# Kernel optimization log

Measured on AMD Instinct MI355X. Metric: run time of the kernel, lower is better.

## Reference

```python
import jax, jax.numpy as jnp
import numpy as np

G = 131072      # number of agent groups (batched graphs)
N_AGENTS = 6    # 5 search parties + 1 helicopter, fully-connected graph per group
D_IN = 64       # input_dim
H = 64          # hidden_dim (conv1 out)
GH = 64         # gnn_hidden (conv2 out, MLP hidden)
OUT = 2         # actor action dim
N_TYPES = 2     # agent types: search party (0), helicopter (1)


def setup_inputs() -> dict:
    key = jax.random.key(0)
    ks = jax.random.split(key, 20)
    s = 0.05
    inp = {
        'obs': jax.random.normal(ks[0], (G, N_AGENTS, D_IN), jnp.float32),
        # SAGEConv('pool') layer 1: fc_pool (in->in), fc_self, fc_neigh, bias
        'Wp1': jax.random.normal(ks[1], (D_IN, D_IN), jnp.float32) * s,
        'bp1': jnp.zeros((D_IN,), jnp.float32),
        'Ws1': jax.random.normal(ks[2], (D_IN, H), jnp.float32) * s,
        'Wn1': jax.random.normal(ks[3], (D_IN, H), jnp.float32) * s,
        'b1': jnp.zeros((H,), jnp.float32),
        # SAGEConv('pool') layer 2
        'Wp2': jax.random.normal(ks[4], (H, H), jnp.float32) * s,
        'bp2': jnp.zeros((H,), jnp.float32),
        'Ws2': jax.random.normal(ks[5], (H, GH), jnp.float32) * s,
        'Wn2': jax.random.normal(ks[6], (H, GH), jnp.float32) * s,
        'b2': jnp.zeros((GH,), jnp.float32),
        # per-agent-type actor MLPs (stacked over type axis t=2)
        'MW1': jax.random.normal(ks[7], (N_TYPES, GH, GH), jnp.float32) * s,
        'Mb1': jnp.zeros((N_TYPES, GH), jnp.float32),
        'MW2': jax.random.normal(ks[8], (N_TYPES, GH, GH), jnp.float32) * s,
        'Mb2': jnp.zeros((N_TYPES, GH), jnp.float32),
        'MW3': jax.random.normal(ks[9], (N_TYPES, GH, GH), jnp.float32) * s,
        'Mb3': jnp.zeros((N_TYPES, GH), jnp.float32),
        'MW4': jax.random.uniform(ks[10], (N_TYPES, GH, OUT), jnp.float32, -0.003, 0.003),
        'Mb4': jnp.zeros((N_TYPES, OUT), jnp.float32),
    }
    return inp


def _sage_pool(x, Wp, bp, Ws, Wn, b):
    # DGL SAGEConv aggregator_type='pool' on a fully-connected graph w/ self loops:
    # neigh_j = max_i relu(fc_pool(x_i)); rst = fc_self(x) + fc_neigh(neigh) + bias
    p = jax.nn.relu(x @ Wp + bp)              # [G, n, din]
    neigh = p.max(axis=1, keepdims=True)      # [G, 1, din] (all nodes are neighbors)
    return x @ Ws + neigh @ Wn + b            # [G, n, dout]


def reference(obs, Wp1, bp1, Ws1, Wn1, b1, Wp2, bp2, Ws2, Wn2, b2,
              MW1, Mb1, MW2, Mb2, MW3, Mb3, MW4, Mb4):
    h = jnp.tanh(_sage_pool(obs, Wp1, bp1, Ws1, Wn1, b1))   # conv1 + Tanh activation
    h = _sage_pool(h, Wp2, bp2, Ws2, Wn2, b2)               # conv2 (no activation)
    res = h.mean(axis=1)                                     # AvgPooling per graph -> [G, GH]
    # per-agent-type MLPs, batched over type axis t
    x = jax.nn.relu(jnp.einsum('gd,tdh->tgh', res, MW1) + Mb1[:, None, :])
    x = jax.nn.relu(jnp.einsum('tgh,thk->tgk', x, MW2) + Mb2[:, None, :])
    x = jax.nn.relu(jnp.einsum('tgh,thk->tgk', x, MW3) + Mb3[:, None, :])
    out_t = jnp.tanh(jnp.einsum('tgh,tho->tgo', x, MW4) + Mb4[:, None, :])  # [T, G, 2]
    agent_types = jnp.array([0, 0, 0, 0, 0, 1])  # 5 search parties + 1 helicopter
    return jnp.transpose(out_t[agent_types], (1, 0, 2))     # [G, 6, 2]
```

## Files before the change

### kernel.cpp

```cpp
#include <hip/hip_runtime.h>
#include <math.h>


typedef _Float16 f16;
typedef _Float16 half8_t __attribute__((ext_vector_type(8)));
typedef float    float4_t __attribute__((ext_vector_type(4)));

#define NW 8
#define SLABF (16*68)
#define LDS_PAD_F 17920

__device__ __forceinline__ int swz_off(int n, int k) {
    return n * 64 + (((k >> 3) ^ (n & 7)) << 3) + (k & 7);
}

__device__ __forceinline__ float fast_tanh(float x) {
    float e = __expf(2.0f * x);
    return 1.0f - 2.0f / (e + 1.0f);
}

__device__ __forceinline__ float4_t max4(float4_t a, float4_t b) {
    float4_t r;
    r[0] = fmaxf(a[0], b[0]); r[1] = fmaxf(a[1], b[1]);
    r[2] = fmaxf(a[2], b[2]); r[3] = fmaxf(a[3], b[3]);
    return r;
}

__device__ __forceinline__ float4_t bcast4(float v) {
    float4_t r; r[0] = v; r[1] = v; r[2] = v; r[3] = v; return r;
}

__global__ void prep_weights(const float* __restrict__ Wp1, const float* __restrict__ Ws1,
                             const float* __restrict__ Wn1, const float* __restrict__ Wp2,
                             const float* __restrict__ Ws2, const float* __restrict__ Wn2,
                             const float* __restrict__ MW1, const float* __restrict__ MW2,
                             const float* __restrict__ MW3, const float* __restrict__ MW4,
                             f16* __restrict__ img)
{
    const int m = blockIdx.x;
    const int tid = threadIdx.x;
    if (m < 12) {
        const float* src;
        switch (m) {
            case 0: src = Wp1; break;  case 1: src = Ws1; break;
            case 2: src = Wn1; break;  case 3: src = Wp2; break;
            case 4: src = Ws2; break;  case 5: src = Wn2; break;
            case 6: src = MW1; break;  case 7: src = MW2; break;
            case 8: src = MW3; break;  case 9: src = MW1 + 4096; break;
            case 10: src = MW2 + 4096; break; default: src = MW3 + 4096; break;
        }
        for (int e = tid; e < 4096; e += 256) {
            const int k = e >> 6, n = e & 63;
            img[m * 4096 + swz_off(n, k)] = (f16)src[e];
        }
    } else {
        for (int e = tid; e < 2048; e += 256) {
            const int ty = e >> 10, rem = e & 1023;
            const int n = rem >> 6, k = rem & 63;
            float v = 0.f;
            if (ty == 0) { if (n < 10) v = MW4[k * 2 + (n & 1)]; }
            else         { if (n == 10 || n == 11) v = MW4[128 + k * 2 + (n & 1)]; }
            img[12 * 4096 + ty * 1024 + swz_off(n, k)] = (f16)v;
        }
    }
}

__global__ __launch_bounds__(512, 2)
void gnn_mfma(const float* __restrict__ obs, const f16* __restrict__ img,
              const float* __restrict__ bp1, const float* __restrict__ b1,
              const float* __restrict__ bp2, const float* __restrict__ b2,
              const float* __restrict__ Mb1, const float* __restrict__ Mb2,
              const float* __restrict__ Mb3, const float* __restrict__ Mb4,
              float* __restrict__ out)
{
    __shared__ __align__(16) float smem[LDS_PAD_F];

    const int tid  = threadIdx.x;
    const int w    = __builtin_amdgcn_readfirstlane(tid >> 6);
    const int l    = tid & 63;
    const int col  = l & 15;
    const int quad = l >> 4;
    float* slab = smem + w * SLABF;

    if (tid == 0) {
        volatile float* guard = smem + NW * SLABF;
        guard[0] = 0.f;
    }

    auto loadB = [&](int baseH, int nt, int kf) -> half8_t {
        const int n = nt * 16 + col;
        const unsigned off = (unsigned)(baseH + n * 64 + (((kf * 4 + quad) ^ (n & 7)) << 3));
        return *(const half8_t*)(img + off);
    };
    auto loadA = [&](int kf) -> half8_t {
        const float4_t x = *(const float4_t*)(slab + col * 68 + kf * 32 + quad * 8);
        const float4_t y = *(const float4_t*)(slab + col * 68 + kf * 32 + quad * 8 + 4);
        half8_t r;
        r[0] = (f16)x[0]; r[1] = (f16)x[1]; r[2] = (f16)x[2]; r[3] = (f16)x[3];
        r[4] = (f16)y[0]; r[5] = (f16)y[1]; r[6] = (f16)y[2]; r[7] = (f16)y[3];
        return r;
    };
    auto storeC = [&](const float4_t v, int nt) {
        #pragma unroll
        for (int r = 0; r < 4; ++r)
            slab[(quad * 4 + r) * 68 + nt * 16 + col] = v[r];
    };

    float bp1v[4], b1v[4], bp2v[4], b2v[4];
    #pragma unroll
    for (int nt = 0; nt < 4; ++nt) {
        bp1v[nt] = bp1[nt * 16 + col];
        b1v[nt]  = b1[nt * 16 + col];
        bp2v[nt] = bp2[nt * 16 + col];
        b2v[nt]  = b2[nt * 16 + col];
    }
    const float mb4v = (col < 10) ? Mb4[col & 1] : Mb4[2 + (col & 1)];

    const int wid = blockIdx.x * NW + w;
    const int g0  = wid * 16;

    half8_t Aobs[6][2];
    const float* orow = obs + ((size_t)(g0 + col) * 6) * 64 + quad * 8;
    #pragma unroll
    for (int a = 0; a < 6; ++a) {
        #pragma unroll
        for (int kf = 0; kf < 2; ++kf) {
            const float4_t x = *(const float4_t*)(orow + a * 64 + kf * 32);
            const float4_t y = *(const float4_t*)(orow + a * 64 + kf * 32 + 4);
            half8_t r;
            r[0] = (f16)x[0]; r[1] = (f16)x[1]; r[2] = (f16)x[2]; r[3] = (f16)x[3];
            r[4] = (f16)y[0]; r[5] = (f16)y[1]; r[6] = (f16)y[2]; r[7] = (f16)y[3];
            Aobs[a][kf] = r;
        }
    }

    half8_t B0[4][2];
    #pragma unroll
    for (int nt = 0; nt < 4; ++nt)
        #pragma unroll
        for (int kf = 0; kf < 2; ++kf) B0[nt][kf] = loadB(0 * 4096, nt, kf);
    float4_t n1[4];
    #pragma unroll
    for (int nt = 0; nt < 4; ++nt) n1[nt] = bcast4(0.f);
    #pragma unroll
    for (int a = 0; a < 6; ++a) {
        #pragma unroll
        for (int nt = 0; nt < 4; ++nt) {
            float4_t acc = bcast4(bp1v[nt]);
            acc = __builtin_amdgcn_mfma_f32_16x16x32_f16(Aobs[a][0], B0[nt][0], acc, 0, 0, 0);
            acc = __builtin_amdgcn_mfma_f32_16x16x32_f16(Aobs[a][1], B0[nt][1], acc, 0, 0, 0);
            n1[nt] = max4(n1[nt], acc);
        }
    }

    #pragma unroll
    for (int nt = 0; nt < 4; ++nt) storeC(n1[nt], nt);
    {
        const half8_t a0 = loadA(0), a1 = loadA(1);
        #pragma unroll
        for (int nt = 0; nt < 4; ++nt) {
            float4_t acc = bcast4(b1v[nt]);
            acc = __builtin_amdgcn_mfma_f32_16x16x32_f16(a0, loadB(2 * 4096, nt, 0), acc, 0, 0, 0);
            acc = __builtin_amdgcn_mfma_f32_16x16x32_f16(a1, loadB(2 * 4096, nt, 1), acc, 0, 0, 0);
            n1[nt] = acc;
        }
    }

    half8_t B1[4][2], B3[4][2];
    #pragma unroll
    for (int nt = 0; nt < 4; ++nt)
        #pragma unroll
        for (int kf = 0; kf < 2; ++kf) {
            B1[nt][kf] = loadB(1 * 4096, nt, kf);
            B3[nt][kf] = loadB(3 * 4096, nt, kf);
        }
    float4_t hbar[4], n2[4];
    #pragma unroll
    for (int nt = 0; nt < 4; ++nt) { hbar[nt] = bcast4(0.f); n2[nt] = bcast4(0.f); }
    #pragma unroll
    for (int a = 0; a < 6; ++a) {
        #pragma unroll
        for (int nt = 0; nt < 4; ++nt) {
            float4_t acc = n1[nt];
            acc = __builtin_amdgcn_mfma_f32_16x16x32_f16(Aobs[a][0], B1[nt][0], acc, 0, 0, 0);
            acc = __builtin_amdgcn_mfma_f32_16x16x32_f16(Aobs[a][1], B1[nt][1], acc, 0, 0, 0);
            #pragma unroll
            for (int r = 0; r < 4; ++r) acc[r] = fast_tanh(acc[r]);
            hbar[nt] += acc;
            storeC(acc, nt);
        }
        const half8_t ha0 = loadA(0), ha1 = loadA(1);
        #pragma unroll
        for (int nt = 0; nt < 4; ++nt) {
            float4_t q = bcast4(bp2v[nt]);
            q = __builtin_amdgcn_mfma_f32_16x16x32_f16(ha0, B3[nt][0], q, 0, 0, 0);
            q = __builtin_amdgcn_mfma_f32_16x16x32_f16(ha1, B3[nt][1], q, 0, 0, 0);
            n2[nt] = max4(n2[nt], q);
        }
    }
    #pragma unroll
    for (int nt = 0; nt < 4; ++nt) hbar[nt] *= (1.0f / 6.0f);

    float4_t rres[4];
    #pragma unroll
    for (int nt = 0; nt < 4; ++nt) storeC(hbar[nt], nt);
    {
        const half8_t a0 = loadA(0), a1 = loadA(1);
        #pragma unroll
        for (int nt = 0; nt < 4; ++nt) {
            float4_t acc = bcast4(b2v[nt]);
            acc = __builtin_amdgcn_mfma_f32_16x16x32_f16(a0, loadB(4 * 4096, nt, 0), acc, 0, 0, 0);
            acc = __builtin_amdgcn_mfma_f32_16x16x32_f16(a1, loadB(4 * 4096, nt, 1), acc, 0, 0, 0);
            rres[nt] = acc;
        }
    }
    #pragma unroll
    for (int nt = 0; nt < 4; ++nt) storeC(n2[nt], nt);
    {
        const half8_t a0 = loadA(0), a1 = loadA(1);
        #pragma unroll
        for (int nt = 0; nt < 4; ++nt) {
            rres[nt] = __builtin_amdgcn_mfma_f32_16x16x32_f16(a0, loadB(5 * 4096, nt, 0), rres[nt], 0, 0, 0);
            rres[nt] = __builtin_amdgcn_mfma_f32_16x16x32_f16(a1, loadB(5 * 4096, nt, 1), rres[nt], 0, 0, 0);
        }
    }

    half8_t x3f[2][2];
    #pragma unroll
    for (int ty = 0; ty < 2; ++ty) {
        #pragma unroll
        for (int nt = 0; nt < 4; ++nt) storeC(rres[nt], nt);
        half8_t xa0 = loadA(0), xa1 = loadA(1);
        #pragma unroll
        for (int layer = 0; layer < 3; ++layer) {
            const int baseH = (6 + ty * 3 + layer) * 4096;
            const float* Mb = (layer == 0 ? Mb1 : layer == 1 ? Mb2 : Mb3) + ty * 64;
            #pragma unroll
            for (int nt = 0; nt < 4; ++nt) {
                float4_t acc = bcast4(Mb[nt * 16 + col]);
                acc = __builtin_amdgcn_mfma_f32_16x16x32_f16(xa0, loadB(baseH, nt, 0), acc, 0, 0, 0);
                acc = __builtin_amdgcn_mfma_f32_16x16x32_f16(xa1, loadB(baseH, nt, 1), acc, 0, 0, 0);
                acc = max4(acc, bcast4(0.f));
                storeC(acc, nt);
            }
            xa0 = loadA(0); xa1 = loadA(1);
        }
        x3f[ty][0] = xa0; x3f[ty][1] = xa1;
    }

    float4_t d = bcast4(0.f);
    d = __builtin_amdgcn_mfma_f32_16x16x32_f16(x3f[0][0], loadB(12 * 4096, 0, 0), d, 0, 0, 0);
    d = __builtin_amdgcn_mfma_f32_16x16x32_f16(x3f[0][1], loadB(12 * 4096, 0, 1), d, 0, 0, 0);
    d = __builtin_amdgcn_mfma_f32_16x16x32_f16(x3f[1][0], loadB(12 * 4096 + 1024, 0, 0), d, 0, 0, 0);
    d = __builtin_amdgcn_mfma_f32_16x16x32_f16(x3f[1][1], loadB(12 * 4096 + 1024, 0, 1), d, 0, 0, 0);

    if (col < 12) {
        #pragma unroll
        for (int r = 0; r < 4; ++r) {
            const float v = fast_tanh(d[r] + mb4v);
            out[(size_t)(g0 + quad * 4 + r) * 12 + col] = v;
        }
    }
}

extern "C" void kernel_launch(void* const* d_in, const int* in_sizes, int n_in,
                              void* d_out, int out_size, void* d_ws, size_t ws_size,
                              hipStream_t stream)
{
    const float* obs = (const float*)d_in[0];
    const float* Wp1 = (const float*)d_in[1];
    const float* bp1 = (const float*)d_in[2];
    const float* Ws1 = (const float*)d_in[3];
    const float* Wn1 = (const float*)d_in[4];
    const float* b1  = (const float*)d_in[5];
    const float* Wp2 = (const float*)d_in[6];
    const float* bp2 = (const float*)d_in[7];
    const float* Ws2 = (const float*)d_in[8];
    const float* Wn2 = (const float*)d_in[9];
    const float* b2  = (const float*)d_in[10];
    const float* MW1 = (const float*)d_in[11];
    const float* Mb1 = (const float*)d_in[12];
    const float* MW2 = (const float*)d_in[13];
    const float* Mb2 = (const float*)d_in[14];
    const float* MW3 = (const float*)d_in[15];
    const float* Mb3 = (const float*)d_in[16];
    const float* MW4 = (const float*)d_in[17];
    const float* Mb4 = (const float*)d_in[18];
    float* out = (float*)d_out;
    f16* img = (f16*)d_ws;

    hipLaunchKernelGGL(prep_weights, dim3(13), dim3(256), 0, stream,
                       Wp1, Ws1, Wn1, Wp2, Ws2, Wn2, MW1, MW2, MW3, MW4, img);
    hipLaunchKernelGGL(gnn_mfma, dim3(1024), dim3(512), 0, stream,
                       obs, img, bp1, b1, bp2, b2, Mb1, Mb2, Mb3, Mb4, out);
}
```

Baseline: 370.8 us.

## Cut register pressure by streaming obs and weight fragments instead of holding them

Drops the register-resident array of all six agents' obs fragments. Obs rows are now loaded per agent (software-prefetched in conv1, re-read in conv2), and the B1/B3 weight fragments are fetched from global memory inside rolled loops instead of being held in registers. Float-to-half conversion switches to packed round-toward-zero instructions. The aim is lower VGPR use and higher occupancy, at the cost of re-reading obs and weights from cache, plus rolled-loop overhead and a rounding-mode change.

```diff
diff --git a/kernel.cpp b/kernel.cpp
--- a/kernel.cpp
+++ b/kernel.cpp
@@ -3,6 +3,7 @@
 
 
 typedef _Float16 f16;
+typedef __fp16   fp16x2_t __attribute__((ext_vector_type(2)));
 typedef _Float16 half8_t __attribute__((ext_vector_type(8)));
 typedef float    float4_t __attribute__((ext_vector_type(4)));
 
@@ -28,6 +29,17 @@
 
 __device__ __forceinline__ float4_t bcast4(float v) {
     float4_t r; r[0] = v; r[1] = v; r[2] = v; r[3] = v; return r;
+}
+
+__device__ __forceinline__ half8_t pk8(float4_t x, float4_t y) {
+    fp16x2_t p0 = __builtin_amdgcn_cvt_pkrtz(x[0], x[1]);
+    fp16x2_t p1 = __builtin_amdgcn_cvt_pkrtz(x[2], x[3]);
+    fp16x2_t p2 = __builtin_amdgcn_cvt_pkrtz(y[0], y[1]);
+    fp16x2_t p3 = __builtin_amdgcn_cvt_pkrtz(y[2], y[3]);
+    half8_t r;
+    r[0] = (f16)p0[0]; r[1] = (f16)p0[1]; r[2] = (f16)p1[0]; r[3] = (f16)p1[1];
+    r[4] = (f16)p2[0]; r[5] = (f16)p2[1]; r[6] = (f16)p3[0]; r[7] = (f16)p3[1];
+    return r;
 }
 
 __global__ void prep_weights(const float* __restrict__ Wp1, const float* __restrict__ Ws1,
@@ -93,12 +105,8 @@
         return *(const half8_t*)(img + off);
     };
     auto loadA = [&](int kf) -> half8_t {
-        const float4_t x = *(const float4_t*)(slab + col * 68 + kf * 32 + quad * 8);
-        const float4_t y = *(const float4_t*)(slab + col * 68 + kf * 32 + quad * 8 + 4);
-        half8_t r;
-        r[0] = (f16)x[0]; r[1] = (f16)x[1]; r[2] = (f16)x[2]; r[3] = (f16)x[3];
-        r[4] = (f16)y[0]; r[5] = (f16)y[1]; r[6] = (f16)y[2]; r[7] = (f16)y[3];
-        return r;
+        const float* p = slab + col * 68 + kf * 32 + quad * 8;
+        return pk8(*(const float4_t*)p, *(const float4_t*)(p + 4));
     };
     auto storeC = [&](const float4_t v, int nt) {
         #pragma unroll
@@ -118,38 +126,40 @@
 
     const int wid = blockIdx.x * NW + w;
     const int g0  = wid * 16;
-
-    half8_t Aobs[6][2];
     const float* orow = obs + ((size_t)(g0 + col) * 6) * 64 + quad * 8;
-    #pragma unroll
-    for (int a = 0; a < 6; ++a) {
-        #pragma unroll
-        for (int kf = 0; kf < 2; ++kf) {
-            const float4_t x = *(const float4_t*)(orow + a * 64 + kf * 32);
-            const float4_t y = *(const float4_t*)(orow + a * 64 + kf * 32 + 4);
-            half8_t r;
-            r[0] = (f16)x[0]; r[1] = (f16)x[1]; r[2] = (f16)x[2]; r[3] = (f16)x[3];
-            r[4] = (f16)y[0]; r[5] = (f16)y[1]; r[6] = (f16)y[2]; r[7] = (f16)y[3];
-            Aobs[a][kf] = r;
-        }
-    }
 
     half8_t B0[4][2];
     #pragma unroll
-    for (int nt = 0; nt < 4; ++nt)
-        #pragma unroll
-        for (int kf = 0; kf < 2; ++kf) B0[nt][kf] = loadB(0 * 4096, nt, kf);
+    for (int nt = 0; nt < 4; ++nt) {
+        B0[nt][0] = loadB(0, nt, 0);
+        B0[nt][1] = loadB(0, nt, 1);
+    }
     float4_t n1[4];
     #pragma unroll
     for (int nt = 0; nt < 4; ++nt) n1[nt] = bcast4(0.f);
-    #pragma unroll
-    for (int a = 0; a < 6; ++a) {
-        #pragma unroll
-        for (int nt = 0; nt < 4; ++nt) {
-            float4_t acc = bcast4(bp1v[nt]);
-            acc = __builtin_amdgcn_mfma_f32_16x16x32_f16(Aobs[a][0], B0[nt][0], acc, 0, 0, 0);
-            acc = __builtin_amdgcn_mfma_f32_16x16x32_f16(Aobs[a][1], B0[nt][1], acc, 0, 0, 0);
-            n1[nt] = max4(n1[nt], acc);
+    {
+        float4_t px0 = *(const float4_t*)(orow);
+        float4_t px1 = *(const float4_t*)(orow + 4);
+        float4_t py0 = *(const float4_t*)(orow + 32);
+        float4_t py1 = *(const float4_t*)(orow + 36);
+        #pragma unroll 1
+        for (int a = 0; a < 6; ++a) {
+            const half8_t A0 = pk8(px0, px1);
+            const half8_t A1 = pk8(py0, py1);
+            if (a < 5) {
+                const float* p = orow + (a + 1) * 64;
+                px0 = *(const float4_t*)(p);
+                px1 = *(const float4_t*)(p + 4);
+                py0 = *(const float4_t*)(p + 32);
+                py1 = *(const float4_t*)(p + 36);
+            }
+            #pragma unroll
+            for (int nt = 0; nt < 4; ++nt) {
+                float4_t acc = bcast4(bp1v[nt]);
+                acc = __builtin_amdgcn_mfma_f32_16x16x32_f16(A0, B0[nt][0], acc, 0, 0, 0);
+                acc = __builtin_amdgcn_mfma_f32_16x16x32_f16(A1, B0[nt][1], acc, 0, 0, 0);
+                n1[nt] = max4(n1[nt], acc);
+            }
         }
     }
 
@@ -166,24 +176,21 @@
         }
     }
 
-    half8_t B1[4][2], B3[4][2];
-    #pragma unroll
-    for (int nt = 0; nt < 4; ++nt)
-        #pragma unroll
-        for (int kf = 0; kf < 2; ++kf) {
-            B1[nt][kf] = loadB(1 * 4096, nt, kf);
-            B3[nt][kf] = loadB(3 * 4096, nt, kf);
-        }
     float4_t hbar[4], n2[4];
     #pragma unroll
     for (int nt = 0; nt < 4; ++nt) { hbar[nt] = bcast4(0.f); n2[nt] = bcast4(0.f); }
-    #pragma unroll
+    #pragma unroll 1
     for (int a = 0; a < 6; ++a) {
+        int b1b = 1 * 4096, b3b = 3 * 4096;
+        asm volatile("" : "+s"(b1b), "+s"(b3b));
+        const float* p = orow + a * 64;
+        const half8_t A0 = pk8(*(const float4_t*)(p),      *(const float4_t*)(p + 4));
+        const half8_t A1 = pk8(*(const float4_t*)(p + 32), *(const float4_t*)(p + 36));
         #pragma unroll
         for (int nt = 0; nt < 4; ++nt) {
             float4_t acc = n1[nt];
-            acc = __builtin_amdgcn_mfma_f32_16x16x32_f16(Aobs[a][0], B1[nt][0], acc, 0, 0, 0);
-            acc = __builtin_amdgcn_mfma_f32_16x16x32_f16(Aobs[a][1], B1[nt][1], acc, 0, 0, 0);
+            acc = __builtin_amdgcn_mfma_f32_16x16x32_f16(A0, loadB(b1b, nt, 0), acc, 0, 0, 0);
+            acc = __builtin_amdgcn_mfma_f32_16x16x32_f16(A1, loadB(b1b, nt, 1), acc, 0, 0, 0);
             #pragma unroll
             for (int r = 0; r < 4; ++r) acc[r] = fast_tanh(acc[r]);
             hbar[nt] += acc;
@@ -193,8 +200,8 @@
         #pragma unroll
         for (int nt = 0; nt < 4; ++nt) {
             float4_t q = bcast4(bp2v[nt]);
-            q = __builtin_amdgcn_mfma_f32_16x16x32_f16(ha0, B3[nt][0], q, 0, 0, 0);
-            q = __builtin_amdgcn_mfma_f32_16x16x32_f16(ha1, B3[nt][1], q, 0, 0, 0);
+            q = __builtin_amdgcn_mfma_f32_16x16x32_f16(ha0, loadB(b3b, nt, 0), q, 0, 0, 0);
+            q = __builtin_amdgcn_mfma_f32_16x16x32_f16(ha1, loadB(b3b, nt, 1), q, 0, 0, 0);
             n2[nt] = max4(n2[nt], q);
         }
     }
@@ -231,15 +238,16 @@
         #pragma unroll
         for (int nt = 0; nt < 4; ++nt) storeC(rres[nt], nt);
         half8_t xa0 = loadA(0), xa1 = loadA(1);
-        #pragma unroll
+        #pragma unroll 1
         for (int layer = 0; layer < 3; ++layer) {
-            const int baseH = (6 + ty * 3 + layer) * 4096;
+            int bb = (6 + ty * 3 + layer) * 4096;
+            asm volatile("" : "+s"(bb));
             const float* Mb = (layer == 0 ? Mb1 : layer == 1 ? Mb2 : Mb3) + ty * 64;
             #pragma unroll
             for (int nt = 0; nt < 4; ++nt) {
                 float4_t acc = bcast4(Mb[nt * 16 + col]);
-                acc = __builtin_amdgcn_mfma_f32_16x16x32_f16(xa0, loadB(baseH, nt, 0), acc, 0, 0, 0);
-                acc = __builtin_amdgcn_mfma_f32_16x16x32_f16(xa1, loadB(baseH, nt, 1), acc, 0, 0, 0);
+                acc = __builtin_amdgcn_mfma_f32_16x16x32_f16(xa0, loadB(bb, nt, 0), acc, 0, 0, 0);
+                acc = __builtin_amdgcn_mfma_f32_16x16x32_f16(xa1, loadB(bb, nt, 1), acc, 0, 0, 0);
                 acc = max4(acc, bcast4(0.f));
                 storeC(acc, nt);
             }
```

Measured after the change: 396.9 us. +7.0%, slower.

## Use transposed 16x16x16 MFMA chaining to keep activations in registers, dropping LDS staging

Applied to the files above, without the earlier changes.

Switches from 16x16x32 MFMAs with activations as the A operand to 16x16x16 MFMAs with weights as A and activations as B. The accumulator output layout then matches the next layer's B-operand layout, so intermediate activations pass between layers in registers instead of going through per-wave LDS store/load round trips. Weights are pre-packed into an MFMA-fragment order for coalesced per-lane loads, obs is reloaded per agent rather than held in registers, and outputs are written as float4. The cost is twice as many MFMA instructions and more global/L2 weight loads inside the loops, traded for no LDS traffic and lower register pressure.

```diff
diff --git a/kernel.cpp b/kernel.cpp
--- a/kernel.cpp
+++ b/kernel.cpp
@@ -3,16 +3,14 @@
 
 
 typedef _Float16 f16;
-typedef _Float16 half8_t __attribute__((ext_vector_type(8)));
+typedef __fp16   fp16x2_t __attribute__((ext_vector_type(2)));
+typedef _Float16 half4_t  __attribute__((ext_vector_type(4)));
 typedef float    float4_t __attribute__((ext_vector_type(4)));
 
 #define NW 8
-#define SLABF (16*68)
 #define LDS_PAD_F 17920
 
-__device__ __forceinline__ int swz_off(int n, int k) {
-    return n * 64 + (((k >> 3) ^ (n & 7)) << 3) + (k & 7);
-}
+#define MFMA16(A,B,C) __builtin_amdgcn_mfma_f32_16x16x16f16((A),(B),(C),0,0,0)
 
 __device__ __forceinline__ float fast_tanh(float x) {
     float e = __expf(2.0f * x);
@@ -28,6 +26,14 @@
 
 __device__ __forceinline__ float4_t bcast4(float v) {
     float4_t r; r[0] = v; r[1] = v; r[2] = v; r[3] = v; return r;
+}
+
+__device__ __forceinline__ half4_t cvt4(float4_t v) {
+    fp16x2_t p0 = __builtin_amdgcn_cvt_pkrtz(v[0], v[1]);
+    fp16x2_t p1 = __builtin_amdgcn_cvt_pkrtz(v[2], v[3]);
+    half4_t r;
+    r[0] = (f16)p0[0]; r[1] = (f16)p0[1]; r[2] = (f16)p1[0]; r[3] = (f16)p1[1];
+    return r;
 }
 
 __global__ void prep_weights(const float* __restrict__ Wp1, const float* __restrict__ Ws1,
@@ -50,17 +56,22 @@
             case 10: src = MW2 + 4096; break; default: src = MW3 + 4096; break;
         }
         for (int e = tid; e < 4096; e += 256) {
-            const int k = e >> 6, n = e & 63;
-            img[m * 4096 + swz_off(n, k)] = (f16)src[e];
+            const int mt = e >> 10, o = e & 1023;
+            const int kt = o >> 8, lane = (o >> 2) & 63, j = e & 3;
+            const int k = kt * 16 + (lane >> 4) * 4 + j;
+            const int n = mt * 16 + (lane & 15);
+            img[m * 4096 + e] = (f16)src[k * 64 + n];
         }
     } else {
         for (int e = tid; e < 2048; e += 256) {
-            const int ty = e >> 10, rem = e & 1023;
-            const int n = rem >> 6, k = rem & 63;
+            const int ty = e >> 10, o = e & 1023;
+            const int kt = o >> 8, lane = (o >> 2) & 63, j = e & 3;
+            const int k = kt * 16 + (lane >> 4) * 4 + j;
+            const int mm = lane & 15;
             float v = 0.f;
-            if (ty == 0) { if (n < 10) v = MW4[k * 2 + (n & 1)]; }
-            else         { if (n == 10 || n == 11) v = MW4[128 + k * 2 + (n & 1)]; }
-            img[12 * 4096 + ty * 1024 + swz_off(n, k)] = (f16)v;
+            if (ty == 0) { if (mm < 10) v = MW4[k * 2 + (mm & 1)]; }
+            else         { if (mm == 10 || mm == 11) v = MW4[128 + k * 2 + (mm & 1)]; }
+            img[12 * 4096 + e] = (f16)v;
         }
     }
 }
@@ -74,192 +85,183 @@
               float* __restrict__ out)
 {
     __shared__ __align__(16) float smem[LDS_PAD_F];
-
     const int tid  = threadIdx.x;
+    if (tid == 0) { volatile float* g = smem; g[0] = 0.f; }
+
     const int w    = __builtin_amdgcn_readfirstlane(tid >> 6);
     const int l    = tid & 63;
     const int col  = l & 15;
     const int quad = l >> 4;
-    float* slab = smem + w * SLABF;
-
-    if (tid == 0) {
-        volatile float* guard = smem + NW * SLABF;
-        guard[0] = 0.f;
-    }
-
-    auto loadB = [&](int baseH, int nt, int kf) -> half8_t {
-        const int n = nt * 16 + col;
-        const unsigned off = (unsigned)(baseH + n * 64 + (((kf * 4 + quad) ^ (n & 7)) << 3));
-        return *(const half8_t*)(img + off);
-    };
-    auto loadA = [&](int kf) -> half8_t {
-        const float4_t x = *(const float4_t*)(slab + col * 68 + kf * 32 + quad * 8);
-        const float4_t y = *(const float4_t*)(slab + col * 68 + kf * 32 + quad * 8 + 4);
-        half8_t r;
-        r[0] = (f16)x[0]; r[1] = (f16)x[1]; r[2] = (f16)x[2]; r[3] = (f16)x[3];
-        r[4] = (f16)y[0]; r[5] = (f16)y[1]; r[6] = (f16)y[2]; r[7] = (f16)y[3];
-        return r;
-    };
-    auto storeC = [&](const float4_t v, int nt) {
-        #pragma unroll
-        for (int r = 0; r < 4; ++r)
-            slab[(quad * 4 + r) * 68 + nt * 16 + col] = v[r];
-    };
-
-    float bp1v[4], b1v[4], bp2v[4], b2v[4];
-    #pragma unroll
-    for (int nt = 0; nt < 4; ++nt) {
-        bp1v[nt] = bp1[nt * 16 + col];
-        b1v[nt]  = b1[nt * 16 + col];
-        bp2v[nt] = bp2[nt * 16 + col];
-        b2v[nt]  = b2[nt * 16 + col];
-    }
-    const float mb4v = (col < 10) ? Mb4[col & 1] : Mb4[2 + (col & 1)];
 
     const int wid = blockIdx.x * NW + w;
     const int g0  = wid * 16;
 
-    half8_t Aobs[6][2];
-    const float* orow = obs + ((size_t)(g0 + col) * 6) * 64 + quad * 8;
+    const float* orow = obs + (size_t)(g0 + col) * 384 + quad * 4;
+
+    auto loadW = [&](int baseH, int mt, int kt) -> half4_t {
+        return *(const half4_t*)(img + baseH + (mt * 4 + kt) * 256 + l * 4);
+    };
+    auto loadObs = [&](const float* ob_, int a, int kt) -> half4_t {
+        return cvt4(*(const float4_t*)(ob_ + a * 64 + kt * 16));
+    };
+
+    half4_t Wp1f[4][4];
+    #pragma unroll
+    for (int mt = 0; mt < 4; ++mt)
+        #pragma unroll
+        for (int kt = 0; kt < 4; ++kt) Wp1f[mt][kt] = loadW(0, mt, kt);
+    float4_t bq[4];
+    #pragma unroll
+    for (int mt = 0; mt < 4; ++mt)
+        bq[mt] = *(const float4_t*)(bp1 + mt * 16 + quad * 4);
+
+    float4_t n1[4];
+    #pragma unroll
+    for (int mt = 0; mt < 4; ++mt) n1[mt] = bcast4(0.f);
     #pragma unroll
     for (int a = 0; a < 6; ++a) {
-        #pragma unroll
-        for (int kf = 0; kf < 2; ++kf) {
-            const float4_t x = *(const float4_t*)(orow + a * 64 + kf * 32);
-            const float4_t y = *(const float4_t*)(orow + a * 64 + kf * 32 + 4);
-            half8_t r;
-            r[0] = (f16)x[0]; r[1] = (f16)x[1]; r[2] = (f16)x[2]; r[3] = (f16)x[3];
-            r[4] = (f16)y[0]; r[5] = (f16)y[1]; r[6] = (f16)y[2]; r[7] = (f16)y[3];
-            Aobs[a][kf] = r;
-        }
-    }
-
-    half8_t B0[4][2];
-    #pragma unroll
-    for (int nt = 0; nt < 4; ++nt)
-        #pragma unroll
-        for (int kf = 0; kf < 2; ++kf) B0[nt][kf] = loadB(0 * 4096, nt, kf);
-    float4_t n1[4];
-    #pragma unroll
-    for (int nt = 0; nt < 4; ++nt) n1[nt] = bcast4(0.f);
+        half4_t ob[4];
+        #pragma unroll
+        for (int kt = 0; kt < 4; ++kt) ob[kt] = loadObs(orow, a, kt);
+        #pragma unroll
+        for (int mt = 0; mt < 4; ++mt) {
+            float4_t acc = bq[mt];
+            #pragma unroll
+            for (int kt = 0; kt < 4; ++kt)
+                acc = MFMA16(Wp1f[mt][kt], ob[kt], acc);
+            n1[mt] = max4(n1[mt], acc);
+        }
+    }
+
+    half4_t n1h[4];
+    #pragma unroll
+    for (int kt = 0; kt < 4; ++kt) n1h[kt] = cvt4(n1[kt]);
+    float4_t c[4];
+    {
+        int bW = 2 * 4096;
+        asm volatile("" : "+s"(bW));
+        #pragma unroll
+        for (int mt = 0; mt < 4; ++mt) {
+            float4_t acc = *(const float4_t*)(b1 + mt * 16 + quad * 4);
+            #pragma unroll
+            for (int kt = 0; kt < 4; ++kt)
+                acc = MFMA16(loadW(bW, mt, kt), n1h[kt], acc);
+            c[mt] = acc;
+        }
+    }
+
+    float4_t bp2q[4];
+    #pragma unroll
+    for (int mt = 0; mt < 4; ++mt)
+        bp2q[mt] = *(const float4_t*)(bp2 + mt * 16 + quad * 4);
+    size_t orp = (size_t)orow;
+    asm volatile("" : "+v"(orp));
+    const float* orow2 = (const float*)orp;
+
+    float4_t hbar[4], n2[4];
+    #pragma unroll
+    for (int mt = 0; mt < 4; ++mt) { hbar[mt] = bcast4(0.f); n2[mt] = bcast4(0.f); }
     #pragma unroll
     for (int a = 0; a < 6; ++a) {
-        #pragma unroll
-        for (int nt = 0; nt < 4; ++nt) {
-            float4_t acc = bcast4(bp1v[nt]);
-            acc = __builtin_amdgcn_mfma_f32_16x16x32_f16(Aobs[a][0], B0[nt][0], acc, 0, 0, 0);
-            acc = __builtin_amdgcn_mfma_f32_16x16x32_f16(Aobs[a][1], B0[nt][1], acc, 0, 0, 0);
-            n1[nt] = max4(n1[nt], acc);
-        }
-    }
-
-    #pragma unroll
-    for (int nt = 0; nt < 4; ++nt) storeC(n1[nt], nt);
+        int bWs = 1 * 4096, bWp = 3 * 4096;
+        asm volatile("" : "+s"(bWs), "+s"(bWp));
+        half4_t ob[4];
+        #pragma unroll
+        for (int kt = 0; kt < 4; ++kt) ob[kt] = loadObs(orow2, a, kt);
+        half4_t hh[4];
+        #pragma unroll
+        for (int mt = 0; mt < 4; ++mt) {
+            float4_t acc = c[mt];
+            #pragma unroll
+            for (int kt = 0; kt < 4; ++kt)
+                acc = MFMA16(loadW(bWs, mt, kt), ob[kt], acc);
+            #pragma unroll
+            for (int r = 0; r < 4; ++r) acc[r] = fast_tanh(acc[r]);
+            hbar[mt] += acc;
+            hh[mt] = cvt4(acc);
+        }
+        #pragma unroll
+        for (int mt = 0; mt < 4; ++mt) {
+            float4_t q = bp2q[mt];
+            #pragma unroll
+            for (int kt = 0; kt < 4; ++kt)
+                q = MFMA16(loadW(bWp, mt, kt), hh[kt], q);
+            n2[mt] = max4(n2[mt], q);
+        }
+    }
+    #pragma unroll
+    for (int mt = 0; mt < 4; ++mt) hbar[mt] *= (1.0f / 6.0f);
+
+    half4_t hbh[4], n2h[4];
+    #pragma unroll
+    for (int kt = 0; kt < 4; ++kt) { hbh[kt] = cvt4(hbar[kt]); n2h[kt] = cvt4(n2[kt]); }
+    float4_t rr[4];
     {
-        const half8_t a0 = loadA(0), a1 = loadA(1);
-        #pragma unroll
-        for (int nt = 0; nt < 4; ++nt) {
-            float4_t acc = bcast4(b1v[nt]);
-            acc = __builtin_amdgcn_mfma_f32_16x16x32_f16(a0, loadB(2 * 4096, nt, 0), acc, 0, 0, 0);
-            acc = __builtin_amdgcn_mfma_f32_16x16x32_f16(a1, loadB(2 * 4096, nt, 1), acc, 0, 0, 0);
-            n1[nt] = acc;
-        }
-    }
-
-    half8_t B1[4][2], B3[4][2];
-    #pragma unroll
-    for (int nt = 0; nt < 4; ++nt)
-        #pragma unroll
-        for (int kf = 0; kf < 2; ++kf) {
-            B1[nt][kf] = loadB(1 * 4096, nt, kf);
-            B3[nt][kf] = loadB(3 * 4096, nt, kf);
-        }
-    float4_t hbar[4], n2[4];
-    #pragma unroll
-    for (int nt = 0; nt < 4; ++nt) { hbar[nt] = bcast4(0.f); n2[nt] = bcast4(0.f); }
-    #pragma unroll
-    for (int a = 0; a < 6; ++a) {
-        #pragma unroll
-        for (int nt = 0; nt < 4; ++nt) {
-            float4_t acc = n1[nt];
-            acc = __builtin_amdgcn_mfma_f32_16x16x32_f16(Aobs[a][0], B1[nt][0], acc, 0, 0, 0);
-            acc = __builtin_amdgcn_mfma_f32_16x16x32_f16(Aobs[a][1], B1[nt][1], acc, 0, 0, 0);
-            #pragma unroll
-            for (int r = 0; r < 4; ++r) acc[r] = fast_tanh(acc[r]);
-            hbar[nt] += acc;
-            storeC(acc, nt);
-        }
-        const half8_t ha0 = loadA(0), ha1 = loadA(1);
-        #pragma unroll
-        for (int nt = 0; nt < 4; ++nt) {
-            float4_t q = bcast4(bp2v[nt]);
-            q = __builtin_amdgcn_mfma_f32_16x16x32_f16(ha0, B3[nt][0], q, 0, 0, 0);
-            q = __builtin_amdgcn_mfma_f32_16x16x32_f16(ha1, B3[nt][1], q, 0, 0, 0);
-            n2[nt] = max4(n2[nt], q);
-        }
-    }
-    #pragma unroll
-    for (int nt = 0; nt < 4; ++nt) hbar[nt] *= (1.0f / 6.0f);
-
-    float4_t rres[4];
-    #pragma unroll
-    for (int nt = 0; nt < 4; ++nt) storeC(hbar[nt], nt);
+        int b4 = 4 * 4096, b5 = 5 * 4096;
+        asm volatile("" : "+s"(b4), "+s"(b5));
+        #pragma unroll
+        for (int mt = 0; mt < 4; ++mt) {
+            float4_t acc = *(const float4_t*)(b2 + mt * 16 + quad * 4);
+            #pragma unroll
+            for (int kt = 0; kt < 4; ++kt)
+                acc = MFMA16(loadW(b4, mt, kt), hbh[kt], acc);
+            #pragma unroll
+            for (int kt = 0; kt < 4; ++kt)
+                acc = MFMA16(loadW(b5, mt, kt), n2h[kt], acc);
+            rr[mt] = acc;
+        }
+    }
+
+    half4_t x3h[2][4];
+    #pragma unroll
+    for (int ty = 0; ty < 2; ++ty) {
+        half4_t xh[4];
+        #pragma unroll
+        for (int kt = 0; kt < 4; ++kt) xh[kt] = cvt4(rr[kt]);
+        #pragma unroll
+        for (int layer = 0; layer < 3; ++layer) {
+            int bb = (6 + ty * 3 + layer) * 4096;
+            asm volatile("" : "+s"(bb));
+            const float* Mb = (layer == 0 ? Mb1 : layer == 1 ? Mb2 : Mb3) + ty * 64;
+            float4_t nx[4];
+            #pragma unroll
+            for (int mt = 0; mt < 4; ++mt) {
+                float4_t acc = *(const float4_t*)(Mb + mt * 16 + quad * 4);
+                #pragma unroll
+                for (int kt = 0; kt < 4; ++kt)
+                    acc = MFMA16(loadW(bb, mt, kt), xh[kt], acc);
+                nx[mt] = max4(acc, bcast4(0.f));
+            }
+            #pragma unroll
+            for (int kt = 0; kt < 4; ++kt) xh[kt] = cvt4(nx[kt]);
+        }
+        #pragma unroll
+        for (int kt = 0; kt < 4; ++kt) x3h[ty][kt] = xh[kt];
+    }
+
+    float4_t d = bcast4(0.f);
     {
-        const half8_t a0 = loadA(0), a1 = loadA(1);
-        #pragma unroll
-        for (int nt = 0; nt < 4; ++nt) {
-            float4_t acc = bcast4(b2v[nt]);
-            acc = __builtin_amdgcn_mfma_f32_16x16x32_f16(a0, loadB(4 * 4096, nt, 0), acc, 0, 0, 0);
-            acc = __builtin_amdgcn_mfma_f32_16x16x32_f16(a1, loadB(4 * 4096, nt, 1), acc, 0, 0, 0);
-            rres[nt] = acc;
-        }
-    }
-    #pragma unroll
-    for (int nt = 0; nt < 4; ++nt) storeC(n2[nt], nt);
-    {
-        const half8_t a0 = loadA(0), a1 = loadA(1);
-        #pragma unroll
-        for (int nt = 0; nt < 4; ++nt) {
-            rres[nt] = __builtin_amdgcn_mfma_f32_16x16x32_f16(a0, loadB(5 * 4096, nt, 0), rres[nt], 0, 0, 0);
-            rres[nt] = __builtin_amdgcn_mfma_f32_16x16x32_f16(a1, loadB(5 * 4096, nt, 1), rres[nt], 0, 0, 0);
-        }
-    }
-
-    half8_t x3f[2][2];
-    #pragma unroll
-    for (int ty = 0; ty < 2; ++ty) {
-        #pragma unroll
-        for (int nt = 0; nt < 4; ++nt) storeC(rres[nt], nt);
-        half8_t xa0 = loadA(0), xa1 = loadA(1);
-        #pragma unroll
-        for (int layer = 0; layer < 3; ++layer) {
-            const int baseH = (6 + ty * 3 + layer) * 4096;
-            const float* Mb = (layer == 0 ? Mb1 : layer == 1 ? Mb2 : Mb3) + ty * 64;
-            #pragma unroll
-            for (int nt = 0; nt < 4; ++nt) {
-                float4_t acc = bcast4(Mb[nt * 16 + col]);
-                acc = __builtin_amdgcn_mfma_f32_16x16x32_f16(xa0, loadB(baseH, nt, 0), acc, 0, 0, 0);
-                acc = __builtin_amdgcn_mfma_f32_16x16x32_f16(xa1, loadB(baseH, nt, 1), acc, 0, 0, 0);
-                acc = max4(acc, bcast4(0.f));
-                storeC(acc, nt);
-            }
-            xa0 = loadA(0); xa1 = loadA(1);
-        }
-        x3f[ty][0] = xa0; x3f[ty][1] = xa1;
-    }
-
-    float4_t d = bcast4(0.f);
-    d = __builtin_amdgcn_mfma_f32_16x16x32_f16(x3f[0][0], loadB(12 * 4096, 0, 0), d, 0, 0, 0);
-    d = __builtin_amdgcn_mfma_f32_16x16x32_f16(x3f[0][1], loadB(12 * 4096, 0, 1), d, 0, 0, 0);
-    d = __builtin_amdgcn_mfma_f32_16x16x32_f16(x3f[1][0], loadB(12 * 4096 + 1024, 0, 0), d, 0, 0, 0);
-    d = __builtin_amdgcn_mfma_f32_16x16x32_f16(x3f[1][1], loadB(12 * 4096 + 1024, 0, 1), d, 0, 0, 0);
-
-    if (col < 12) {
+        int bh = 12 * 4096;
+        asm volatile("" : "+s"(bh));
+        #pragma unroll
+        for (int kt = 0; kt < 4; ++kt)
+            d = MFMA16(loadW(bh, 0, kt), x3h[0][kt], d);
+        #pragma unroll
+        for (int kt = 0; kt < 4; ++kt)
+            d = MFMA16(loadW(bh + 1024, 0, kt), x3h[1][kt], d);
+    }
+
+    if (quad < 3) {
+        const float m00 = Mb4[0], m01 = Mb4[1], m10 = Mb4[2], m11 = Mb4[3];
+        float4_t v;
         #pragma unroll
         for (int r = 0; r < 4; ++r) {
-            const float v = fast_tanh(d[r] + mb4v);
-            out[(size_t)(g0 + quad * 4 + r) * 12 + col] = v;
-        }
+            const int slot = quad * 4 + r;
+            const float mb = (slot < 10) ? ((r & 1) ? m01 : m00)
+                                         : ((r & 1) ? m11 : m10);
+            v[r] = fast_tanh(d[r] + mb);
+        }
+        *(float4_t*)(out + (size_t)(g0 + col) * 12 + quad * 4) = v;
     }
 }
 
```

After: 470.6 us. 26.9% more time.
